# Kernel tuning notes

Hardware: AMD Instinct MI355X
Metric: run time of the kernel (lower is better)

Reference implementation:

```python
import jax, jax.numpy as jnp
import numpy as np

B, D, H = 262144, 250, 100  # batch, input_length, hidden_length


def setup_inputs() -> dict:
    key = jax.random.key(0)
    ks = jax.random.split(key, 20)
    s_in = 1.0 / np.sqrt(D)
    s_h = 1.0 / np.sqrt(H)
    inp = {
        "x": jax.random.normal(ks[0], (B, D), jnp.float32),
        "h_prev": jax.random.normal(ks[1], (B, H), jnp.float32),
        "h_shared_prev": jax.random.normal(ks[2], (B, H), jnp.float32),
        # shared nn.GRUCell(D, H) params (torch layout: weight_ih [3H, D], weight_hh [3H, H])
        "Wi": jax.random.uniform(ks[3], (3 * H, D), jnp.float32, -s_in, s_in),
        "Wh": jax.random.uniform(ks[4], (3 * H, H), jnp.float32, -s_h, s_h),
        "bi": jax.random.uniform(ks[5], (3 * H,), jnp.float32, -s_h, s_h),
        "bh": jax.random.uniform(ks[6], (3 * H,), jnp.float32, -s_h, s_h),
        # task-specific bias-free linears, torch nn.Linear layout [out, in]
        "W_z": jax.random.uniform(ks[7], (H, D), jnp.float32, -s_in, s_in),
        "U_z": jax.random.uniform(ks[8], (H, H), jnp.float32, -s_h, s_h),
        "Us_z": jax.random.uniform(ks[9], (H, H), jnp.float32, -s_h, s_h),
        "W_r": jax.random.uniform(ks[10], (H, D), jnp.float32, -s_in, s_in),
        "U_r": jax.random.uniform(ks[11], (H, H), jnp.float32, -s_h, s_h),
        "Us_r": jax.random.uniform(ks[12], (H, H), jnp.float32, -s_h, s_h),
        "W_hn": jax.random.uniform(ks[13], (H, D), jnp.float32, -s_in, s_in),
        "U_hn": jax.random.uniform(ks[14], (H, H), jnp.float32, -s_h, s_h),
        "Us_hn": jax.random.uniform(ks[15], (H, H), jnp.float32, -s_h, s_h),
    }
    return inp


def _shared_gru_cell(x, h, Wi, Wh, bi, bh):
    # standard torch nn.GRUCell math
    gi = x @ Wi.T + bi          # [B, 3H]
    gh = h @ Wh.T + bh          # [B, 3H]
    i_r, i_z, i_n = jnp.split(gi, 3, axis=-1)
    h_r, h_z, h_n = jnp.split(gh, 3, axis=-1)
    r = jax.nn.sigmoid(i_r + h_r)
    z = jax.nn.sigmoid(i_z + h_z)
    n = jnp.tanh(i_n + r * h_n)
    return (1.0 - z) * n + z * h


def reference(x, h_prev, h_shared_prev, Wi, Wh, bi, bh,
              W_z, U_z, Us_z, W_r, U_r, Us_r, W_hn, U_hn, Us_hn):
    h_shared_new = _shared_gru_cell(x, h_shared_prev, Wi, Wh, bi, bh)
    z = jax.nn.sigmoid(x @ W_z.T + h_prev @ U_z.T + h_shared_new @ Us_z.T)
    r = jax.nn.sigmoid(x @ W_r.T + h_prev @ U_r.T + h_shared_new @ Us_r.T)
    nm = jnp.tanh(x @ W_hn.T + r * (h_prev @ U_hn.T) + h_shared_new @ Us_hn.T)
    h_new = (1.0 - z) * nm + z * h_prev
    return h_new
```

## Files before the change

kernel.cpp:

```cpp
#include <hip/hip_runtime.h>
#include <stdint.h>

#define D_IN 250
#define H_DIM 100
#define RPW 32
#define NTHREADS 256
#define BM (4*RPW)

#define P2_FRAG 252
#define TOTAL_E ((252 + 336) * 512)

typedef __bf16 bf16x8 __attribute__((ext_vector_type(8)));
typedef float f32x4 __attribute__((ext_vector_type(4)));

static __device__ __forceinline__ uint16_t f2bf(float f) {
  uint32_t u = __builtin_bit_cast(uint32_t, f);
  u = (u + 0x7FFFu + ((u >> 16) & 1u)) >> 16;
  return (uint16_t)u;
}
static __device__ __forceinline__ float bf2f(uint16_t h) {
  uint32_t u = ((uint32_t)h) << 16;
  return __builtin_bit_cast(float, u);
}
static __device__ __forceinline__ float sigmoidf_(float x) {
  return 1.0f / (1.0f + __expf(-x));
}
static __device__ __forceinline__ float tanhf_(float x) {
  return 2.0f / (1.0f + __expf(-2.0f * x)) - 1.0f;
}

__global__ void prepack_kernel(const float* __restrict__ Wi, const float* __restrict__ Wh,
                               const float* __restrict__ W_z, const float* __restrict__ U_z,
                               const float* __restrict__ Us_z, const float* __restrict__ W_r,
                               const float* __restrict__ U_r, const float* __restrict__ Us_r,
                               const float* __restrict__ W_hn, const float* __restrict__ U_hn,
                               const float* __restrict__ Us_hn, const float* __restrict__ bi,
                               const float* __restrict__ bh, uint16_t* __restrict__ ws) {
  int idx = blockIdx.x * blockDim.x + threadIdx.x;
  if (idx >= TOTAL_E) return;
  int f = idx >> 9;
  int a = idx & 511;
  int lane = a >> 3, j = a & 7;
  int kloc = ((lane >> 4) << 3) + j;
  int cl = lane & 15;
  float val = 0.f;
  if (f < P2_FRAG) {
    int g = f % 3, ks = (f / 3) % 12, t = f / 36;
    int c = t * 16 + cl;
    if (c < H_DIM) {
      if (ks < 8) {
        int k = ks * 32 + kloc;
        if (k < D_IN)       val = Wi[(size_t)(g * H_DIM + c) * D_IN + k];
        else if (k == D_IN) val = bi[g * H_DIM + c];
      } else {
        int k = (ks - 8) * 32 + kloc;
        if (k < H_DIM)       val = Wh[(size_t)(g * H_DIM + c) * H_DIM + k];
        else if (k == H_DIM) val = bh[g * H_DIM + c];
      }
    }
  } else {
    int f2 = f - P2_FRAG;
    int g = f2 % 3, ks = (f2 / 3) % 16, t = f2 / 48;
    int c = t * 16 + cl;
    if (c < H_DIM) {
      if (ks < 8) {
        int k = ks * 32 + kloc;
        const float* W = g == 0 ? W_z : g == 1 ? W_r : W_hn;
        if (k < D_IN) val = W[(size_t)c * D_IN + k];
      } else if (ks < 12) {
        int k = (ks - 8) * 32 + kloc;
        const float* W = g == 0 ? U_z : g == 1 ? U_r : U_hn;
        if (k < H_DIM) val = W[(size_t)c * H_DIM + k];
      } else {
        int k = (ks - 12) * 32 + kloc;
        const float* W = g == 0 ? Us_z : g == 1 ? Us_r : Us_hn;
        if (k < H_DIM) val = W[(size_t)c * H_DIM + k];
      }
    }
  }
  ws[idx] = f2bf(val);
}

static __device__ __forceinline__ bf16x8 xfrag(const float* __restrict__ xr, int ks, int q) {
  int c0 = ks * 32 + q * 8;
  bf16x8 a;
  if (c0 < 248) {
    #pragma unroll
    for (int i = 0; i < 4; ++i) {
      float2 f = *(const float2*)(xr + c0 + 2 * i);
      a[2 * i] = (__bf16)f.x; a[2 * i + 1] = (__bf16)f.y;
    }
  } else {
    float2 f = *(const float2*)(xr + 248);
    a[0] = (__bf16)f.x; a[1] = (__bf16)f.y; a[2] = (__bf16)1.0f;
    a[3] = (__bf16)0.0f; a[4] = (__bf16)0.0f; a[5] = (__bf16)0.0f;
    a[6] = (__bf16)0.0f; a[7] = (__bf16)0.0f;
  }
  return a;
}
static __device__ __forceinline__ bf16x8 hfrag(const float* __restrict__ hr, int ks, int q, float bias) {
  int c0 = ks * 32 + q * 8;
  bf16x8 a;
  #pragma unroll
  for (int i = 0; i < 8; ++i) a[i] = (__bf16)0.0f;
  if (c0 <= 88) {
    #pragma unroll
    for (int i = 0; i < 4; ++i) {
      float2 f = *(const float2*)(hr + c0 + 2 * i);
      a[2 * i] = (__bf16)f.x; a[2 * i + 1] = (__bf16)f.y;
    }
  } else if (c0 == 96) {
    float2 f0 = *(const float2*)(hr + 96);
    float2 f1 = *(const float2*)(hr + 98);
    a[0] = (__bf16)f0.x; a[1] = (__bf16)f0.y; a[2] = (__bf16)f1.x; a[3] = (__bf16)f1.y;
    a[4] = (__bf16)bias;
  }
  return a;
}

#define MFMA(A, B, C) __builtin_amdgcn_mfma_f32_16x16x32_bf16((A), (B), (C), 0, 0, 0)

typedef const __attribute__((address_space(1))) unsigned int* gp1_t;
typedef __attribute__((address_space(3))) unsigned int* lp3_t;

static __device__ __forceinline__ void issue3(const uint16_t* gsrc0, uint16_t* lslot) {
  #pragma unroll
  for (int g = 0; g < 3; ++g) {
    __builtin_amdgcn_global_load_lds((gp1_t)(gsrc0 + g * 512), (lp3_t)(lslot + g * 512), 16, 0, 0);
  }
}
#define WAIT_VM9  asm volatile("s_waitcnt vmcnt(9)" ::: "memory")
#define WAIT_LGKM0 asm volatile("s_waitcnt lgkmcnt(0)" ::: "memory")

__global__ __launch_bounds__(NTHREADS, 2) void gru_fused(
    const float* __restrict__ x, const float* __restrict__ hp_g,
    const float* __restrict__ hs_g, const uint16_t* __restrict__ ws,
    float* __restrict__ out) {
  __shared__ __align__(16) uint16_t ldsT[4 * RPW * 128];
  __shared__ __align__(16) uint16_t ldsRing[4 * 4 * 1536];

  const int tid = threadIdx.x;
  const int lane = tid & 63, wid = tid >> 6;
  const int q = lane >> 4, cl = lane & 15;
  const int rowbase = blockIdx.x * BM + wid * RPW;
  uint16_t* lT = ldsT + wid * (RPW * 128);
  uint16_t* ring = ldsRing + wid * (4 * 1536);
  const uint16_t* wsl = ws + lane * 8;

  bf16x8 xa[2][8], ha[2][4], pa[2][4];
  #pragma unroll
  for (int h = 0; h < 2; ++h) {
    const float* xr = x + (size_t)(rowbase + h * 16 + cl) * D_IN;
    #pragma unroll
    for (int ks = 0; ks < 8; ++ks) xa[h][ks] = xfrag(xr, ks, q);
    const float* hr = hs_g + (size_t)(rowbase + h * 16 + cl) * H_DIM;
    #pragma unroll
    for (int ks = 0; ks < 4; ++ks) ha[h][ks] = hfrag(hr, ks, q, 1.0f);
    const float* pr = hp_g + (size_t)(rowbase + h * 16 + cl) * H_DIM;
    #pragma unroll
    for (int ks = 0; ks < 4; ++ks) pa[h][ks] = hfrag(pr, ks, q, 0.0f);
  }

  #pragma unroll
  for (int h = 0; h < 2; ++h) {
    int row = h * 16 + cl;
    #pragma unroll
    for (int ks = 0; ks < 4; ++ks) {
      int bo = row * 256 + (((ks * 64) + q * 16) ^ ((row & 7) << 4));
      *(bf16x8*)((char*)lT + bo) = ha[h][ks];
    }
  }

  issue3(wsl + 0 * 512, ring + 0 * 1536);
  issue3(wsl + 3 * 512, ring + 1 * 1536);
  issue3(wsl + 6 * 512, ring + 2 * 1536);

  #pragma unroll 1
  for (int t = 0; t < 7; ++t) {
    f32x4 aR[2], aZ[2], aNi[2], aNh[2];
    #pragma unroll
    for (int h = 0; h < 2; ++h) { aR[h] = (f32x4)(0.f); aZ[h] = (f32x4)(0.f); aNi[h] = (f32x4)(0.f); aNh[h] = (f32x4)(0.f); }
    #pragma unroll
    for (int ks = 0; ks < 12; ++ks) {
      int fidn;
      if (ks < 9)      fidn = t * 36 + (ks + 3) * 3;
      else if (t < 6)  fidn = (t + 1) * 36 + (ks - 9) * 3;
      else             fidn = P2_FRAG + (ks - 9) * 3;
      WAIT_LGKM0;
      issue3(wsl + (size_t)fidn * 512, ring + ((ks + 3) & 3) * 1536);
      WAIT_VM9;
      const uint16_t* sp = ring + (ks & 3) * 1536 + lane * 8;
      bf16x8 b0 = *(const bf16x8*)(sp);
      bf16x8 b1 = *(const bf16x8*)(sp + 512);
      bf16x8 b2 = *(const bf16x8*)(sp + 1024);
      #pragma unroll
      for (int h = 0; h < 2; ++h) {
        bf16x8 av = (ks < 8) ? xa[h][ks] : ha[h][ks - 8];
        aR[h] = MFMA(av, b0, aR[h]);
        aZ[h] = MFMA(av, b1, aZ[h]);
        if (ks < 8) aNi[h] = MFMA(av, b2, aNi[h]);
        else        aNh[h] = MFMA(av, b2, aNh[h]);
      }
    }
    int c = t * 16 + cl;
    #pragma unroll
    for (int h = 0; h < 2; ++h) {
      #pragma unroll
      for (int r = 0; r < 4; ++r) {
        int row = h * 16 + q * 4 + r;
        int bo = row * 256 + ((c * 2) ^ ((row & 7) << 4));
        float hsp = bf2f(*(const uint16_t*)((const char*)lT + bo));
        float rr = sigmoidf_(aR[h][r]);
        float zz = sigmoidf_(aZ[h][r]);
        float nn = tanhf_(aNi[h][r] + rr * aNh[h][r]);
        float hsn = (1.f - zz) * nn + zz * hsp;
        *(uint16_t*)((char*)lT + bo) = f2bf(hsn);
      }
    }
  }

  bf16x8 na[2][4];
  #pragma unroll
  for (int h = 0; h < 2; ++h) {
    int row = h * 16 + cl;
    #pragma unroll
    for (int ks = 0; ks < 4; ++ks) {
      int bo = row * 256 + (((ks * 64) + q * 16) ^ ((row & 7) << 4));
      na[h][ks] = *(const bf16x8*)((const char*)lT + bo);
    }
  }
  WAIT_LGKM0;
  #pragma unroll
  for (int h = 0; h < 2; ++h) {
    int row = h * 16 + cl;
    #pragma unroll
    for (int ks = 0; ks < 4; ++ks) {
      int bo = row * 256 + (((ks * 64) + q * 16) ^ ((row & 7) << 4));
      *(bf16x8*)((char*)lT + bo) = pa[h][ks];
    }
  }

  #pragma unroll 1
  for (int t = 0; t < 7; ++t) {
    f32x4 aZ[2], aR[2], aNa[2], aNb[2];
    #pragma unroll
    for (int h = 0; h < 2; ++h) { aZ[h] = (f32x4)(0.f); aR[h] = (f32x4)(0.f); aNa[h] = (f32x4)(0.f); aNb[h] = (f32x4)(0.f); }
    #pragma unroll
    for (int ks = 0; ks < 16; ++ks) {
      int fidn;
      if (ks < 13)     fidn = P2_FRAG + t * 48 + (ks + 3) * 3;
      else if (t < 6)  fidn = P2_FRAG + (t + 1) * 48 + (ks - 13) * 3;
      else             fidn = P2_FRAG + 6 * 48 + 45;
      WAIT_LGKM0;
      issue3(wsl + (size_t)fidn * 512, ring + ((ks + 3) & 3) * 1536);
      WAIT_VM9;
      const uint16_t* sp = ring + (ks & 3) * 1536 + lane * 8;
      bf16x8 b0 = *(const bf16x8*)(sp);
      bf16x8 b1 = *(const bf16x8*)(sp + 512);
      bf16x8 b2 = *(const bf16x8*)(sp + 1024);
      #pragma unroll
      for (int h = 0; h < 2; ++h) {
        bf16x8 av = (ks < 8) ? xa[h][ks] : (ks < 12) ? pa[h][ks - 8] : na[h][ks - 12];
        aZ[h] = MFMA(av, b0, aZ[h]);
        aR[h] = MFMA(av, b1, aR[h]);
        if (ks < 8)       aNa[h] = MFMA(av, b2, aNa[h]);
        else if (ks < 12) aNb[h] = MFMA(av, b2, aNb[h]);
        else              aNa[h] = MFMA(av, b2, aNa[h]);
      }
    }
    int c = t * 16 + cl;
    bool valid = c < H_DIM;
    #pragma unroll
    for (int h = 0; h < 2; ++h) {
      #pragma unroll
      for (int r = 0; r < 4; ++r) {
        int row = h * 16 + q * 4 + r;
        int bo = row * 256 + ((c * 2) ^ ((row & 7) << 4));
        float hpv = bf2f(*(const uint16_t*)((const char*)lT + bo));
        float z2 = sigmoidf_(aZ[h][r]);
        float r2 = sigmoidf_(aR[h][r]);
        float nm = tanhf_(aNa[h][r] + r2 * aNb[h][r]);
        float hnew = (1.f - z2) * nm + z2 * hpv;
        if (valid) out[(size_t)(rowbase + row) * H_DIM + c] = hnew;
      }
    }
  }
}

extern "C" void kernel_launch(void* const* d_in, const int* in_sizes, int n_in,
                              void* d_out, int out_size, void* d_ws, size_t ws_size,
                              hipStream_t stream) {
  const float* x    = (const float*)d_in[0];
  const float* h_p  = (const float*)d_in[1];
  const float* h_s  = (const float*)d_in[2];
  const float* Wi   = (const float*)d_in[3];
  const float* Wh   = (const float*)d_in[4];
  const float* bi   = (const float*)d_in[5];
  const float* bh   = (const float*)d_in[6];
  const float* W_z  = (const float*)d_in[7];
  const float* U_z  = (const float*)d_in[8];
  const float* Us_z = (const float*)d_in[9];
  const float* W_r  = (const float*)d_in[10];
  const float* U_r  = (const float*)d_in[11];
  const float* Us_r = (const float*)d_in[12];
  const float* W_hn = (const float*)d_in[13];
  const float* U_hn = (const float*)d_in[14];
  const float* Us_hn= (const float*)d_in[15];
  uint16_t* ws = (uint16_t*)d_ws;
  float* out = (float*)d_out;

  int rows = in_sizes[0] / D_IN;
  prepack_kernel<<<(TOTAL_E + 255) / 256, 256, 0, stream>>>(
      Wi, Wh, W_z, U_z, Us_z, W_r, U_r, Us_r, W_hn, U_hn, Us_hn, bi, bh, ws);
  gru_fused<<<rows / BM, NTHREADS, 0, stream>>>(x, h_p, h_s, ws, out);
}
```

Measured before the change: 325.4 us.

## Share one block-wide weight ring across waves with barrier-synchronised cooperative prefetch

Replaces the per-wave private 4-slot weight ring, where each wave loaded all three fragments itself, with a single block-shared 8-slot ring. Three waves each load one fragment per step, six steps ahead, and a block barrier after every k-step publishes the data. This cuts redundant global/L2 weight traffic and LDS footprint by sharing weight fragments among the four waves. The cost is a block barrier on every k-step, which couples the waves and can stall MFMA issue.

```diff
diff --git a/kernel.cpp b/kernel.cpp
--- a/kernel.cpp
+++ b/kernel.cpp
@@ -123,28 +123,25 @@
 typedef const __attribute__((address_space(1))) unsigned int* gp1_t;
 typedef __attribute__((address_space(3))) unsigned int* lp3_t;
 
-static __device__ __forceinline__ void issue3(const uint16_t* gsrc0, uint16_t* lslot) {
-  #pragma unroll
-  for (int g = 0; g < 3; ++g) {
-    __builtin_amdgcn_global_load_lds((gp1_t)(gsrc0 + g * 512), (lp3_t)(lslot + g * 512), 16, 0, 0);
-  }
-}
-#define WAIT_VM9  asm volatile("s_waitcnt vmcnt(9)" ::: "memory")
+static __device__ __forceinline__ void gload(const uint16_t* gsrc, uint16_t* ldst) {
+  __builtin_amdgcn_global_load_lds((gp1_t)gsrc, (lp3_t)ldst, 16, 0, 0);
+}
+#define WAIT_VM5   asm volatile("s_waitcnt vmcnt(5)" ::: "memory")
 #define WAIT_LGKM0 asm volatile("s_waitcnt lgkmcnt(0)" ::: "memory")
+#define BAR        do { __builtin_amdgcn_s_barrier(); __builtin_amdgcn_sched_barrier(0); } while (0)
 
 __global__ __launch_bounds__(NTHREADS, 2) void gru_fused(
     const float* __restrict__ x, const float* __restrict__ hp_g,
     const float* __restrict__ hs_g, const uint16_t* __restrict__ ws,
     float* __restrict__ out) {
   __shared__ __align__(16) uint16_t ldsT[4 * RPW * 128];
-  __shared__ __align__(16) uint16_t ldsRing[4 * 4 * 1536];
+  __shared__ __align__(16) uint16_t ring[8 * 1536];
 
   const int tid = threadIdx.x;
   const int lane = tid & 63, wid = tid >> 6;
   const int q = lane >> 4, cl = lane & 15;
   const int rowbase = blockIdx.x * BM + wid * RPW;
   uint16_t* lT = ldsT + wid * (RPW * 128);
-  uint16_t* ring = ldsRing + wid * (4 * 1536);
   const uint16_t* wsl = ws + lane * 8;
 
   bf16x8 xa[2][8], ha[2][4], pa[2][4];
@@ -171,9 +168,13 @@
     }
   }
 
-  issue3(wsl + 0 * 512, ring + 0 * 1536);
-  issue3(wsl + 3 * 512, ring + 1 * 1536);
-  issue3(wsl + 6 * 512, ring + 2 * 1536);
+  if (wid < 3) {
+    #pragma unroll
+    for (int s = 0; s < 6; ++s)
+      gload(wsl + (size_t)(s * 3 + wid) * 512, ring + s * 1536 + wid * 512);
+    WAIT_VM5;
+  }
+  BAR;
 
   #pragma unroll 1
   for (int t = 0; t < 7; ++t) {
@@ -182,17 +183,16 @@
     for (int h = 0; h < 2; ++h) { aR[h] = (f32x4)(0.f); aZ[h] = (f32x4)(0.f); aNi[h] = (f32x4)(0.f); aNh[h] = (f32x4)(0.f); }
     #pragma unroll
     for (int ks = 0; ks < 12; ++ks) {
-      int fidn;
-      if (ks < 9)      fidn = t * 36 + (ks + 3) * 3;
-      else if (t < 6)  fidn = (t + 1) * 36 + (ks - 9) * 3;
-      else             fidn = P2_FRAG + (ks - 9) * 3;
-      WAIT_LGKM0;
-      issue3(wsl + (size_t)fidn * 512, ring + ((ks + 3) & 3) * 1536);
-      WAIT_VM9;
-      const uint16_t* sp = ring + (ks & 3) * 1536 + lane * 8;
+      const uint16_t* sp = ring + ((t * 12 + ks) & 7) * 1536 + lane * 8;
       bf16x8 b0 = *(const bf16x8*)(sp);
       bf16x8 b1 = *(const bf16x8*)(sp + 512);
       bf16x8 b2 = *(const bf16x8*)(sp + 1024);
+      if (wid < 3) {
+        int fid = (ks < 6) ? (t * 36 + (ks + 6) * 3)
+                : (t < 6 ? ((t + 1) * 36 + (ks - 6) * 3) : (P2_FRAG + (ks - 6) * 3));
+        gload(wsl + (size_t)(fid + wid) * 512,
+              ring + ((t * 12 + ks + 6) & 7) * 1536 + wid * 512);
+      }
       #pragma unroll
       for (int h = 0; h < 2; ++h) {
         bf16x8 av = (ks < 8) ? xa[h][ks] : ha[h][ks - 8];
@@ -201,6 +201,8 @@
         if (ks < 8) aNi[h] = MFMA(av, b2, aNi[h]);
         else        aNh[h] = MFMA(av, b2, aNh[h]);
       }
+      if (wid < 3) WAIT_VM5;
+      BAR;
     }
     int c = t * 16 + cl;
     #pragma unroll
@@ -247,17 +249,17 @@
     for (int h = 0; h < 2; ++h) { aZ[h] = (f32x4)(0.f); aR[h] = (f32x4)(0.f); aNa[h] = (f32x4)(0.f); aNb[h] = (f32x4)(0.f); }
     #pragma unroll
     for (int ks = 0; ks < 16; ++ks) {
-      int fidn;
-      if (ks < 13)     fidn = P2_FRAG + t * 48 + (ks + 3) * 3;
-      else if (t < 6)  fidn = P2_FRAG + (t + 1) * 48 + (ks - 13) * 3;
-      else             fidn = P2_FRAG + 6 * 48 + 45;
-      WAIT_LGKM0;
-      issue3(wsl + (size_t)fidn * 512, ring + ((ks + 3) & 3) * 1536);
-      WAIT_VM9;
-      const uint16_t* sp = ring + (ks & 3) * 1536 + lane * 8;
+      const uint16_t* sp = ring + ((84 + t * 16 + ks) & 7) * 1536 + lane * 8;
       bf16x8 b0 = *(const bf16x8*)(sp);
       bf16x8 b1 = *(const bf16x8*)(sp + 512);
       bf16x8 b2 = *(const bf16x8*)(sp + 1024);
+      if (wid < 3) {
+        int fid = (ks < 10) ? (P2_FRAG + t * 48 + (ks + 6) * 3)
+                : (t < 6 ? (P2_FRAG + (t + 1) * 48 + (ks - 10) * 3)
+                         : (P2_FRAG + 6 * 48 + 15 * 3));
+        gload(wsl + (size_t)(fid + wid) * 512,
+              ring + ((84 + t * 16 + ks + 6) & 7) * 1536 + wid * 512);
+      }
       #pragma unroll
       for (int h = 0; h < 2; ++h) {
         bf16x8 av = (ks < 8) ? xa[h][ks] : (ks < 12) ? pa[h][ks - 8] : na[h][ks - 12];
@@ -267,6 +269,8 @@
         else if (ks < 12) aNb[h] = MFMA(av, b2, aNb[h]);
         else              aNa[h] = MFMA(av, b2, aNa[h]);
       }
+      if (wid < 3) WAIT_VM5;
+      BAR;
     }
     int c = t * 16 + cl;
     bool valid = c < H_DIM;
```

Measured after the change: 272.0 us. 1.2x faster.
